# Kernel tuning notes

Measured on AMD Instinct MI355X. Metric: run time of the kernel, lower is better.

## Reference

```python
import jax, jax.numpy as jnp
import numpy as np


def _maxpool2x2(t):
    # t: [B, C, H, W] -> [B, C, H//2, W//2]
    b, c, h, w = t.shape
    return t.reshape(b, c, h // 2, 2, w // 2, 2).max(axis=(3, 5))


def setup_inputs() -> dict:
    key = jax.random.key(0)
    ks = jax.random.split(key, 6)
    B, C, H, W = 16, 64, 64, 64
    x = jax.random.normal(ks[0], (B, C, H, W), dtype=jnp.float32)
    # 1x1 conv weights (no bias), stored as [out_ch, in_ch]
    s = 0.05
    W_theta = jax.random.normal(ks[1], (C // 8, C), dtype=jnp.float32) * s
    W_phi = jax.random.normal(ks[2], (C // 8, C), dtype=jnp.float32) * s
    W_g = jax.random.normal(ks[3], (C // 2, C), dtype=jnp.float32) * s
    W_attn = jax.random.normal(ks[4], (C, C // 2), dtype=jnp.float32) * s
    sigma = jnp.ones((1,), dtype=jnp.float32) * 0.5  # nonzero so attn path matters
    return {"x": x, "W_theta": W_theta, "W_phi": W_phi, "W_g": W_g,
            "W_attn": W_attn, "sigma": sigma}


def reference(x, W_theta, W_phi, W_g, W_attn, sigma):
    B, C, H, W = x.shape
    N = H * W
    M = N // 4
    # 1x1 convs are channel matmuls
    theta = jnp.einsum('oc,bchw->bohw', W_theta, x).reshape(B, C // 8, N)      # [B, C/8, N]
    phi = _maxpool2x2(jnp.einsum('oc,bchw->bohw', W_phi, x)).reshape(B, C // 8, M)  # [B, C/8, M]
    attn = jax.nn.softmax(jnp.einsum('bkn,bkm->bnm', theta, phi), axis=-1)    # [B, N, M]
    g = _maxpool2x2(jnp.einsum('oc,bchw->bohw', W_g, x)).reshape(B, C // 2, M)  # [B, C/2, M]
    attn_g = jnp.einsum('bgm,bnm->bgn', g, attn).reshape(B, C // 2, H, W)      # [B, C/2, H, W]
    attn_g = jnp.einsum('oc,bchw->bohw', W_attn, attn_g)                        # [B, C, H, W]
    return x + sigma * attn_g
```

## Files before the change

### kernel.cpp

```cpp
#include <hip/hip_runtime.h>
#include <hip/hip_bf16.h>

#define CC 64
#define NN 4096
#define MM 1024

typedef __attribute__((ext_vector_type(4))) short s4b;
typedef __attribute__((ext_vector_type(4))) float float4v;

__device__ inline unsigned short f2bf(float f) {
    union { float f; unsigned u; } v; v.f = f;
    unsigned r = v.u + 0x7fff + ((v.u >> 16) & 1);
    return (unsigned short)(r >> 16);
}

__device__ inline float4v mfma16(s4b a, s4b b, float4v c) {
#if __has_builtin(__builtin_amdgcn_mfma_f32_16x16x16bf16_1k)
    return __builtin_amdgcn_mfma_f32_16x16x16bf16_1k(a, b, c, 0, 0, 0);
#else
    float4v d;
    asm volatile("v_mfma_f32_16x16x16_bf16 %0, %1, %2, %3"
                 : "=v"(d) : "v"(a), "v"(b), "v"(c));
    return d;
#endif
}

__global__ __launch_bounds__(256) void prep_kernel(
    const float* __restrict__ x,
    const float* __restrict__ Wth,
    const float* __restrict__ Wph,
    const float* __restrict__ Wg,
    unsigned short* __restrict__ thT,
    unsigned short* __restrict__ phiP,
    unsigned short* __restrict__ gP)
{
    __shared__ float wt[64 * 48];
    __shared__ float buf[128 * 49];

    const int tid  = threadIdx.x;
    const int b    = blockIdx.y;
    const int hp   = blockIdx.x;
    const int pix  = tid & 127;
    const int half = tid >> 7;

    for (int idx = tid; idx < 64 * 48; idx += 256) {
        const int c = idx / 48, j = idx % 48;
        float v;
        if (j < 8)       v = Wth[j * 64 + c];
        else if (j < 16) v = Wph[(j - 8) * 64 + c];
        else             v = Wg[(j - 16) * 64 + c];
        wt[c * 48 + j] = v;
    }
    __syncthreads();

    const int n = (2 * hp + (pix >> 6)) * 64 + (pix & 63);
    const float* xb = x + (size_t)b * CC * NN + (size_t)half * 32 * NN + n;

    float acc[48];
#pragma unroll
    for (int j = 0; j < 48; ++j) acc[j] = 0.f;

#pragma unroll
    for (int c0 = 0; c0 < 32; c0 += 16) {
        float xv[16];
#pragma unroll
        for (int u = 0; u < 16; ++u) xv[u] = xb[(size_t)(c0 + u) * NN];
#pragma unroll
        for (int u = 0; u < 16; ++u) {
            const float* wrow = &wt[(half * 32 + c0 + u) * 48];
#pragma unroll
            for (int j = 0; j < 48; ++j) acc[j] += wrow[j] * xv[u];
        }
    }

    if (half == 1) {
#pragma unroll
        for (int j = 0; j < 48; ++j) buf[pix * 49 + j] = acc[j];
    }
    __syncthreads();

    if (half == 0) {
#pragma unroll
        for (int j = 0; j < 48; ++j) acc[j] += buf[pix * 49 + j];
        union { unsigned short s[8]; uint4 v; } pk;
#pragma unroll
        for (int j = 0; j < 8; ++j) pk.s[j] = f2bf(acc[j] * 1.44269504f);
        *(uint4*)&thT[((size_t)b * NN + n) * 8] = pk.v;
#pragma unroll
        for (int j = 0; j < 40; ++j) buf[pix * 49 + j] = acc[8 + j];
    }
    __syncthreads();

    for (int idx = tid; idx < 1280; idx += 256) {
        const int pm = idx & 31;
        const int j  = idx >> 5;
        const int p00 = 2 * pm, p10 = 64 + 2 * pm;
        const float v = fmaxf(fmaxf(buf[p00 * 49 + j], buf[(p00 + 1) * 49 + j]),
                              fmaxf(buf[p10 * 49 + j], buf[(p10 + 1) * 49 + j]));
        const int m = hp * 32 + pm;
        if (j < 8) phiP[((size_t)b * MM + m) * 8 + j] = f2bf(v);
        else       gP[((size_t)b * 32 + (j - 8)) * MM + m] = f2bf(v);
    }
}

__global__ __launch_bounds__(256) void attn_mfma(
    const unsigned short* __restrict__ thT,
    const unsigned short* __restrict__ phiP,
    const unsigned short* __restrict__ gP,
    const float* __restrict__ x,
    const float* __restrict__ Wa,
    const float* __restrict__ sigma,
    float* __restrict__ out)
{
    constexpr int GP = 264;
    constexpr int OP = 36;

    __shared__ __align__(16) union {
        struct {
            unsigned short phi[256 * 8 + 16];
            unsigned short g[32 * GP];
        } m;
        float obar[64 * OP];
    } sh;
    __shared__ __align__(16) float wa_s[64 * 32];

    const int tid  = threadIdx.x;
    const int lane = tid & 63;
    const int wv   = tid >> 6;
    const int c15  = lane & 15;
    const int quad = lane >> 4;
    const int b    = blockIdx.y;
    const int n0   = blockIdx.x * 64;

    for (int i = tid; i < 2048; i += 256) wa_s[i] = Wa[i];

    s4b zero4 = {0, 0, 0, 0};
    s4b bth = zero4;
    if (quad < 2) {
        union { uint2 u; s4b s; } t;
        t.u = *(const uint2*)&thT[((size_t)b * NN + n0 + wv * 16 + c15) * 8 + quad * 4];
        bth = t.s;
    }

    float4v acc0 = {0.f, 0.f, 0.f, 0.f};
    float4v acc1 = {0.f, 0.f, 0.f, 0.f};
    float zacc = 0.f;

    for (int ch = 0; ch < 4; ++ch) {
        __syncthreads();
        *(uint4*)&sh.m.phi[tid * 8] =
            *(const uint4*)&phiP[((size_t)b * MM + ch * 256 + tid) * 8];
        if (tid < 2) {
            uint4 z4; z4.x = z4.y = z4.z = z4.w = 0u;
            *(uint4*)&sh.m.phi[256 * 8 + tid * 8] = z4;
        }
#pragma unroll
        for (int it = 0; it < 4; ++it) {
            const int idx = tid + 256 * it;
            const int row = idx >> 5, c32 = idx & 31;
            *(uint4*)&sh.m.g[row * GP + c32 * 8] =
                *(const uint4*)&gP[((size_t)b * 32 + row) * MM + ch * 256 + c32 * 8];
        }
        __syncthreads();

#pragma unroll 4
        for (int st = 0; st < 16; ++st) {
            const int kb = st * 16;

            union { uint2 u; s4b s; } ap;
            ap.u = *(const uint2*)&sh.m.phi[(kb + c15) * 8 + quad * 4];

            float4v cz = {0.f, 0.f, 0.f, 0.f};
            float4v sc = mfma16(ap.s, bth, cz);

            union { float f; unsigned u; } e0, e1, e2, e3;
            e0.f = __builtin_amdgcn_exp2f(sc[0]);
            e1.f = __builtin_amdgcn_exp2f(sc[1]);
            e2.f = __builtin_amdgcn_exp2f(sc[2]);
            e3.f = __builtin_amdgcn_exp2f(sc[3]);
            zacc += (e0.f + e1.f) + (e2.f + e3.f);
            union { uint2 u; s4b s; } pa;
            pa.u.x = __builtin_amdgcn_perm(e1.u, e0.u, 0x07060302u);
            pa.u.y = __builtin_amdgcn_perm(e3.u, e2.u, 0x07060302u);

            union { uint2 u; s4b s; } bg0, bg1;
            bg0.u = *(const uint2*)&sh.m.g[c15 * GP + kb + quad * 4];
            bg1.u = *(const uint2*)&sh.m.g[(16 + c15) * GP + kb + quad * 4];

            acc0 = mfma16(pa.s, bg0.s, acc0);
            acc1 = mfma16(pa.s, bg1.s, acc1);
        }
    }

    float z = zacc;
    z += __shfl_xor(z, 16, 64);
    z += __shfl_xor(z, 32, 64);
    const float rzq = __builtin_amdgcn_rcpf(z);

    __syncthreads();

#pragma unroll
    for (int r = 0; r < 4; ++r) {
        const float rz = __shfl(rzq, quad * 4 + r, 64);
        const int ql = wv * 16 + quad * 4 + r;
        sh.obar[ql * OP + c15]      = acc0[r] * rz;
        sh.obar[ql * OP + 16 + c15] = acc1[r] * rz;
    }
    __syncthreads();

    {
        const int q  = tid & 63;
        const int og = tid >> 6;
        float a[16];
#pragma unroll
        for (int i = 0; i < 16; ++i) a[i] = 0.f;
        const float4* ob4 = (const float4*)&sh.obar[q * OP];
        const float4* wa4 = (const float4*)wa_s;
#pragma unroll
        for (int g4 = 0; g4 < 8; ++g4) {
            const float4 ob = ob4[g4];
#pragma unroll
            for (int i = 0; i < 16; ++i) {
                const float4 w = wa4[(og * 16 + i) * 8 + g4];
                a[i] += w.x * ob.x + w.y * ob.y + w.z * ob.z + w.w * ob.w;
            }
        }
        const float sg = sigma[0];
#pragma unroll
        for (int i = 0; i < 16; ++i) {
            const size_t oi = ((size_t)b * CC + og * 16 + i) * NN + n0 + q;
            out[oi] = x[oi] + sg * a[i];
        }
    }
}

extern "C" void kernel_launch(void* const* d_in, const int* in_sizes, int n_in,
                              void* d_out, int out_size, void* d_ws, size_t ws_size,
                              hipStream_t stream) {
    const float* x      = (const float*)d_in[0];
    const float* W_th   = (const float*)d_in[1];
    const float* W_ph   = (const float*)d_in[2];
    const float* W_g    = (const float*)d_in[3];
    const float* W_attn = (const float*)d_in[4];
    const float* sigma  = (const float*)d_in[5];
    float* out = (float*)d_out;

    const int B = 16;
    unsigned short* thT  = (unsigned short*)d_ws;
    unsigned short* phiP = thT + (size_t)B * NN * 8;
    unsigned short* gP   = phiP + (size_t)B * MM * 8;

    prep_kernel<<<dim3(32, 16), 256, 0, stream>>>(x, W_th, W_ph, W_g,
                                                  thT, phiP, gP);
    attn_mfma<<<dim3(64, 16), 256, 0, stream>>>(thT, phiP, gP, x,
                                                W_attn, sigma, out);
}
```

Measured before the change: 115.7 us.

## Process 128 query pixels per block to reuse staged phi/g tiles across two query tiles

Each wave now handles two 16-query tiles instead of one, so every phi and g fragment loaded from shared memory feeds twice as many MFMAs. The grid halves to 32x16 blocks, which halves the global-to-LDS staging traffic for phi and g per query. The output projection now computes 32 channels per thread over 128 pixels. In exchange, register pressure and ILP per wave rise, and only 512 blocks remain for 256 CUs, which may hurt occupancy and latency hiding.

```diff
diff --git a/kernel.cpp b/kernel.cpp
--- a/kernel.cpp
+++ b/kernel.cpp
@@ -120,7 +120,7 @@
             unsigned short phi[256 * 8 + 16];
             unsigned short g[32 * GP];
         } m;
-        float obar[64 * OP];
+        float obar[128 * OP];
     } sh;
     __shared__ __align__(16) float wa_s[64 * 32];
 
@@ -130,21 +130,25 @@
     const int c15  = lane & 15;
     const int quad = lane >> 4;
     const int b    = blockIdx.y;
-    const int n0   = blockIdx.x * 64;
+    const int n0   = blockIdx.x * 128;
 
     for (int i = tid; i < 2048; i += 256) wa_s[i] = Wa[i];
 
     s4b zero4 = {0, 0, 0, 0};
-    s4b bth = zero4;
+    s4b th0 = zero4, th1 = zero4;
     if (quad < 2) {
         union { uint2 u; s4b s; } t;
-        t.u = *(const uint2*)&thT[((size_t)b * NN + n0 + wv * 16 + c15) * 8 + quad * 4];
-        bth = t.s;
-    }
-
-    float4v acc0 = {0.f, 0.f, 0.f, 0.f};
-    float4v acc1 = {0.f, 0.f, 0.f, 0.f};
-    float zacc = 0.f;
+        t.u = *(const uint2*)&thT[((size_t)b * NN + n0 + wv * 32 + c15) * 8 + quad * 4];
+        th0 = t.s;
+        t.u = *(const uint2*)&thT[((size_t)b * NN + n0 + wv * 32 + 16 + c15) * 8 + quad * 4];
+        th1 = t.s;
+    }
+
+    float4v acc00 = {0.f, 0.f, 0.f, 0.f};
+    float4v acc01 = {0.f, 0.f, 0.f, 0.f};
+    float4v acc10 = {0.f, 0.f, 0.f, 0.f};
+    float4v acc11 = {0.f, 0.f, 0.f, 0.f};
+    float zacc0 = 0.f, zacc1 = 0.f;
 
     for (int ch = 0; ch < 4; ++ch) {
         __syncthreads();
@@ -171,64 +175,80 @@
             ap.u = *(const uint2*)&sh.m.phi[(kb + c15) * 8 + quad * 4];
 
             float4v cz = {0.f, 0.f, 0.f, 0.f};
-            float4v sc = mfma16(ap.s, bth, cz);
-
-            union { float f; unsigned u; } e0, e1, e2, e3;
-            e0.f = __builtin_amdgcn_exp2f(sc[0]);
-            e1.f = __builtin_amdgcn_exp2f(sc[1]);
-            e2.f = __builtin_amdgcn_exp2f(sc[2]);
-            e3.f = __builtin_amdgcn_exp2f(sc[3]);
-            zacc += (e0.f + e1.f) + (e2.f + e3.f);
-            union { uint2 u; s4b s; } pa;
-            pa.u.x = __builtin_amdgcn_perm(e1.u, e0.u, 0x07060302u);
-            pa.u.y = __builtin_amdgcn_perm(e3.u, e2.u, 0x07060302u);
+            float4v sc0 = mfma16(ap.s, th0, cz);
+            float4v sc1 = mfma16(ap.s, th1, cz);
 
             union { uint2 u; s4b s; } bg0, bg1;
             bg0.u = *(const uint2*)&sh.m.g[c15 * GP + kb + quad * 4];
             bg1.u = *(const uint2*)&sh.m.g[(16 + c15) * GP + kb + quad * 4];
 
-            acc0 = mfma16(pa.s, bg0.s, acc0);
-            acc1 = mfma16(pa.s, bg1.s, acc1);
-        }
-    }
-
-    float z = zacc;
-    z += __shfl_xor(z, 16, 64);
-    z += __shfl_xor(z, 32, 64);
-    const float rzq = __builtin_amdgcn_rcpf(z);
+            union { float f; unsigned u; } e0, e1, e2, e3, f0, f1, f2, f3;
+            e0.f = __builtin_amdgcn_exp2f(sc0[0]);
+            e1.f = __builtin_amdgcn_exp2f(sc0[1]);
+            e2.f = __builtin_amdgcn_exp2f(sc0[2]);
+            e3.f = __builtin_amdgcn_exp2f(sc0[3]);
+            f0.f = __builtin_amdgcn_exp2f(sc1[0]);
+            f1.f = __builtin_amdgcn_exp2f(sc1[1]);
+            f2.f = __builtin_amdgcn_exp2f(sc1[2]);
+            f3.f = __builtin_amdgcn_exp2f(sc1[3]);
+            zacc0 += (e0.f + e1.f) + (e2.f + e3.f);
+            zacc1 += (f0.f + f1.f) + (f2.f + f3.f);
+            union { uint2 u; s4b s; } pa0, pa1;
+            pa0.u.x = __builtin_amdgcn_perm(e1.u, e0.u, 0x07060302u);
+            pa0.u.y = __builtin_amdgcn_perm(e3.u, e2.u, 0x07060302u);
+            pa1.u.x = __builtin_amdgcn_perm(f1.u, f0.u, 0x07060302u);
+            pa1.u.y = __builtin_amdgcn_perm(f3.u, f2.u, 0x07060302u);
+
+            acc00 = mfma16(pa0.s, bg0.s, acc00);
+            acc01 = mfma16(pa0.s, bg1.s, acc01);
+            acc10 = mfma16(pa1.s, bg0.s, acc10);
+            acc11 = mfma16(pa1.s, bg1.s, acc11);
+        }
+    }
+
+    float z0 = zacc0, z1 = zacc1;
+    z0 += __shfl_xor(z0, 16, 64);
+    z0 += __shfl_xor(z0, 32, 64);
+    z1 += __shfl_xor(z1, 16, 64);
+    z1 += __shfl_xor(z1, 32, 64);
+    const float rz0 = __builtin_amdgcn_rcpf(z0);
+    const float rz1 = __builtin_amdgcn_rcpf(z1);
 
     __syncthreads();
 
 #pragma unroll
     for (int r = 0; r < 4; ++r) {
-        const float rz = __shfl(rzq, quad * 4 + r, 64);
-        const int ql = wv * 16 + quad * 4 + r;
-        sh.obar[ql * OP + c15]      = acc0[r] * rz;
-        sh.obar[ql * OP + 16 + c15] = acc1[r] * rz;
+        const float ra = __shfl(rz0, quad * 4 + r, 64);
+        const float rb = __shfl(rz1, quad * 4 + r, 64);
+        const int q0 = wv * 32 + quad * 4 + r;
+        sh.obar[q0 * OP + c15]             = acc00[r] * ra;
+        sh.obar[q0 * OP + 16 + c15]        = acc01[r] * ra;
+        sh.obar[(q0 + 16) * OP + c15]      = acc10[r] * rb;
+        sh.obar[(q0 + 16) * OP + 16 + c15] = acc11[r] * rb;
     }
     __syncthreads();
 
     {
-        const int q  = tid & 63;
-        const int og = tid >> 6;
-        float a[16];
-#pragma unroll
-        for (int i = 0; i < 16; ++i) a[i] = 0.f;
+        const int q  = tid & 127;
+        const int og = tid >> 7;
+        float a[32];
+#pragma unroll
+        for (int i = 0; i < 32; ++i) a[i] = 0.f;
         const float4* ob4 = (const float4*)&sh.obar[q * OP];
         const float4* wa4 = (const float4*)wa_s;
 #pragma unroll
         for (int g4 = 0; g4 < 8; ++g4) {
             const float4 ob = ob4[g4];
 #pragma unroll
-            for (int i = 0; i < 16; ++i) {
-                const float4 w = wa4[(og * 16 + i) * 8 + g4];
+            for (int i = 0; i < 32; ++i) {
+                const float4 w = wa4[(og * 32 + i) * 8 + g4];
                 a[i] += w.x * ob.x + w.y * ob.y + w.z * ob.z + w.w * ob.w;
             }
         }
         const float sg = sigma[0];
 #pragma unroll
-        for (int i = 0; i < 16; ++i) {
-            const size_t oi = ((size_t)b * CC + og * 16 + i) * NN + n0 + q;
+        for (int i = 0; i < 32; ++i) {
+            const size_t oi = ((size_t)b * CC + og * 32 + i) * NN + n0 + q;
             out[oi] = x[oi] + sg * a[i];
         }
     }
@@ -252,6 +272,6 @@
 
     prep_kernel<<<dim3(32, 16), 256, 0, stream>>>(x, W_th, W_ph, W_g,
                                                   thT, phiP, gP);
-    attn_mfma<<<dim3(64, 16), 256, 0, stream>>>(thT, phiP, gP, x,
+    attn_mfma<<<dim3(32, 16), 256, 0, stream>>>(thT, phiP, gP, x,
                                                 W_attn, sigma, out);
 }
```

Result: slower. 122.5 us (+5.9%).
